# Performance work log

Hardware: AMD Instinct MI355X
Metric: run time of the kernel (lower is better)

## Reference

```python
import jax, jax.numpy as jnp
import numpy as np

N = 4096
IN_F = 128
OUT_F = 128
H = 4
D = OUT_F // H  # head_out = 32
SLOPE = 0.2
LN_EPS = 1e-5


def setup_inputs() -> dict:
    key = jax.random.key(0)
    k_x, k_adj, k_W, k_a = jax.random.split(key, 4)
    x = jax.random.normal(k_x, (N, IN_F), dtype=jnp.float32)
    adjacency = jax.random.randint(k_adj, (N, N), 0, 2).astype(jnp.bool_)
    # xavier-uniform-ish init scales
    w_std = float(np.sqrt(2.0 / (IN_F + H * D)))
    a_std = float(np.sqrt(2.0 / (H + 2 * D)))
    W = jax.random.normal(k_W, (H * D, IN_F), dtype=jnp.float32) * w_std  # torch Linear weight layout
    a = jax.random.normal(k_a, (H, 2 * D), dtype=jnp.float32) * a_std
    ln_gamma = jnp.ones((OUT_F,), dtype=jnp.float32)
    ln_beta = jnp.zeros((OUT_F,), dtype=jnp.float32)
    return {"x": x, "adjacency": adjacency, "W": W, "a": a,
            "ln_gamma": ln_gamma, "ln_beta": ln_beta}


def reference(x, adjacency, W, a, ln_gamma, ln_beta):
    # Wx: (N, H, D)
    Wx = (x @ W.T).reshape(N, H, D)
    # e[i,j,h] = leaky_relu( <Wx[i,h], a[h,:D]> + <Wx[j,h], a[h,D:]> )
    # (exact factorization of the original cat([Wx_i, Wx_j]) * a sum)
    alpha_i = jnp.einsum('nhd,hd->nh', Wx, a[:, :D])  # source/i term
    alpha_j = jnp.einsum('nhd,hd->nh', Wx, a[:, D:])  # neighbor/j term
    e = alpha_i[:, None, :] + alpha_j[None, :, :]      # (N, N, H)
    e = jnp.where(e >= 0, e, SLOPE * e)                # LeakyReLU
    e = jnp.where(adjacency[:, :, None], e, -jnp.inf)  # mask non-edges
    attn = jax.nn.softmax(e, axis=1)                   # softmax over j
    out = jnp.einsum('ijh,jhd->ihd', attn, Wx).reshape(N, H * D)
    y = out + x                                        # residual (dims match)
    mu = jnp.mean(y, axis=-1, keepdims=True)
    var = jnp.mean((y - mu) ** 2, axis=-1, keepdims=True)
    return ln_gamma * (y - mu) / jnp.sqrt(var + LN_EPS) + ln_beta
```

## Files before the change

### kernel.cpp

```cpp
#include <hip/hip_runtime.h>
#include <hip/hip_bf16.h>
#include <stdint.h>

#define NN 4096
#define SLOPE 0.2f
#define LOG2E 1.44269504088896340736f

typedef float f32x4 __attribute__((ext_vector_type(4)));
typedef float f32x2 __attribute__((ext_vector_type(2)));
typedef short s16x8 __attribute__((ext_vector_type(8)));
typedef unsigned u32x4 __attribute__((ext_vector_type(4)));

static __device__ __forceinline__ unsigned f32_to_bf16_rne(float f) {
    unsigned u = __builtin_bit_cast(unsigned, f);
    return (u + 0x7FFFu + ((u >> 16) & 1u)) >> 16;
}

__global__ __launch_bounds__(256) void k0_pack(const unsigned* __restrict__ src,
                                               unsigned* __restrict__ bits) {
    __shared__ int s_i32;
    const int t = threadIdx.x;
    if (t == 0) {
        int all_small = 1;
        for (int i = 0; i < 32; ++i) all_small &= (src[i] <= 1u);
        s_i32 = all_small;
    }
    __syncthreads();
    const long o = (long)blockIdx.x * 256 + t;
    unsigned m = 0;
    if (s_i32) {
        const u32x4* p = (const u32x4*)src + o * 8;
        #pragma unroll
        for (int g = 0; g < 8; ++g) {
            u32x4 v = p[g];
            m |= (v.x & 1u) << (g * 4) | (v.y & 1u) << (g * 4 + 1) |
                 (v.z & 1u) << (g * 4 + 2) | (v.w & 1u) << (g * 4 + 3);
        }
    } else {
        const u32x4* p = (const u32x4*)src + o * 2;
        #pragma unroll
        for (int g = 0; g < 2; ++g) {
            u32x4 v = p[g];
            unsigned d[4] = {v.x, v.y, v.z, v.w};
            #pragma unroll
            for (int q = 0; q < 4; ++q)
                #pragma unroll
                for (int b = 0; b < 4; ++b)
                    m |= ((d[q] >> (8 * b)) & 1u) << (g * 16 + q * 4 + b);
        }
    }
    bits[o] = m;
}

__global__ __launch_bounds__(256) void k1_wx(const float* __restrict__ x,
                                             const float* __restrict__ W,
                                             const float* __restrict__ a,
                                             unsigned short* __restrict__ wxb,
                                             float* __restrict__ ai_s,
                                             float* __restrict__ ajT_s) {
    __shared__ unsigned short WL[128 * 136];
    __shared__ unsigned short XL[16 * 136];
    __shared__ float WxF[16 * 132];

    const int t = threadIdx.x;
    const int i0 = blockIdx.x * 16;

    for (int p = t; p < 8192; p += 256) {
        f32x2 w2 = *(const f32x2*)(W + 2 * p);
        unsigned lo = f32_to_bf16_rne(w2.x);
        unsigned hi = f32_to_bf16_rne(w2.y);
        int c = (2 * p) >> 7, k = (2 * p) & 127;
        *(unsigned*)&WL[c * 136 + k] = lo | (hi << 16);
    }
    for (int p = t; p < 1024; p += 256) {
        f32x2 x2 = *(const f32x2*)(x + (long)i0 * 128 + 2 * p);
        unsigned lo = f32_to_bf16_rne(x2.x);
        unsigned hi = f32_to_bf16_rne(x2.y);
        int r = (2 * p) >> 7, k = (2 * p) & 127;
        *(unsigned*)&XL[r * 136 + k] = lo | (hi << 16);
    }
    __syncthreads();

    const int w = t >> 6, l = t & 63, m = l & 15, q = l >> 4;
    f32x4 acc0 = {0.f, 0.f, 0.f, 0.f}, acc1 = {0.f, 0.f, 0.f, 0.f};
    #pragma unroll
    for (int ks = 0; ks < 4; ++ks) {
        s16x8 af = *(const s16x8*)&XL[m * 136 + ks * 32 + q * 8];
        s16x8 b0 = *(const s16x8*)&WL[(w * 32 + m) * 136 + ks * 32 + q * 8];
        s16x8 b1 = *(const s16x8*)&WL[(w * 32 + 16 + m) * 136 + ks * 32 + q * 8];
        acc0 = __builtin_amdgcn_mfma_f32_16x16x32_bf16(af, b0, acc0, 0, 0, 0);
        acc1 = __builtin_amdgcn_mfma_f32_16x16x32_bf16(af, b1, acc1, 0, 0, 0);
    }
    #pragma unroll
    for (int j2 = 0; j2 < 2; ++j2) {
        const int fblk = 2 * w + j2;
        f32x4 acc = j2 ? acc1 : acc0;
        #pragma unroll
        for (int reg = 0; reg < 4; ++reg) {
            float v = acc[reg];
            int row_g = i0 + q * 4 + reg;
            int kl = row_g & 31, jblk = row_g >> 5;
            wxb[(((jblk * 8 + fblk) * 64 + (kl >> 3) * 16 + m) << 3) + (kl & 7)] =
                (unsigned short)f32_to_bf16_rne(v);
            WxF[(q * 4 + reg) * 132 + fblk * 16 + m] = v;
        }
    }
    __syncthreads();
    if (t < 64) {
        int r = t >> 2, h = t & 3;
        float s_i = 0.f, s_j = 0.f;
        const float* ar = a + h * 64;
        #pragma unroll
        for (int d = 0; d < 32; ++d) {
            float wv = WxF[r * 132 + h * 32 + d];
            s_i += wv * ar[d];
            s_j += wv * ar[32 + d];
        }
        ai_s[(i0 + r) * 4 + h] = s_i * LOG2E;
        ajT_s[h * NN + i0 + r] = s_j * LOG2E;
    }
}

__global__ __launch_bounds__(512) void k2_attn(const float* __restrict__ x,
                                               const unsigned* __restrict__ adjbits,
                                               const unsigned short* __restrict__ wxb,
                                               const float* __restrict__ ai_s,
                                               const float* __restrict__ ajT_s,
                                               const float* __restrict__ gamma,
                                               const float* __restrict__ beta,
                                               float* __restrict__ out) {
    __shared__ float C_lds[4][16][32];
    __shared__ float l_lds[4][16];

    const int t = threadIdx.x;
    const int i0 = blockIdx.x * 16;
    const int w = t >> 6, l = t & 63;
    const int h = w & 3, p = w >> 2;
    const int m = l & 15, q = l >> 4;
    const int rg = i0 + m;

    const float ai = ai_s[rg * 4 + h];
    const unsigned* abp = adjbits + (long)rg * 128;
    const float* ajp = ajT_s + h * NN + q * 8;
    const unsigned short* bp = wxb + ((2 * h) * 64 + l) * 8;

    f32x4 acc0 = {0.f, 0.f, 0.f, 0.f}, acc1 = {0.f, 0.f, 0.f, 0.f};
    float lpart = 0.f;

    for (int ks = p; ks < 128; ks += 2) {
        unsigned mq = (abp[ks] >> (q * 8)) & 0xffu;
        f32x4 aj0 = *(const f32x4*)(ajp + ks * 32);
        f32x4 aj1 = *(const f32x4*)(ajp + ks * 32 + 4);
        s16x8 b0 = *(const s16x8*)(bp + ks * 4096);
        s16x8 b1 = *(const s16x8*)(bp + ks * 4096 + 512);

        float ev[8];
        #pragma unroll
        for (int e = 0; e < 8; ++e) {
            float s = ai + (e < 4 ? aj0[e] : aj1[e - 4]);
            s = fmaxf(s, SLOPE * s);
            float ex = __builtin_amdgcn_exp2f(s);
            float msk = (float)((mq >> e) & 1u);
            ex *= msk;
            lpart += ex;
            ev[e] = ex;
        }
        union { s16x8 v; unsigned u[4]; } af;
        #pragma unroll
        for (int pr = 0; pr < 4; ++pr) {
            unsigned e0 = __builtin_bit_cast(unsigned, ev[2 * pr]);
            unsigned e1 = __builtin_bit_cast(unsigned, ev[2 * pr + 1]);
            af.u[pr] = __builtin_amdgcn_perm(e1, e0, 0x07060302);
        }
        acc0 = __builtin_amdgcn_mfma_f32_16x16x32_bf16(af.v, b0, acc0, 0, 0, 0);
        acc1 = __builtin_amdgcn_mfma_f32_16x16x32_bf16(af.v, b1, acc1, 0, 0, 0);
    }

    lpart += __shfl_xor(lpart, 16, 64);
    lpart += __shfl_xor(lpart, 32, 64);

    if (p == 0) {
        #pragma unroll
        for (int reg = 0; reg < 4; ++reg) {
            C_lds[h][q * 4 + reg][m] = acc0[reg];
            C_lds[h][q * 4 + reg][16 + m] = acc1[reg];
        }
        if (l < 16) l_lds[h][l] = lpart;
    }
    __syncthreads();
    if (p == 1) {
        #pragma unroll
        for (int reg = 0; reg < 4; ++reg) {
            C_lds[h][q * 4 + reg][m] += acc0[reg];
            C_lds[h][q * 4 + reg][16 + m] += acc1[reg];
        }
        if (l < 16) l_lds[h][l] += lpart;
    }
    __syncthreads();

    {
        const int r = t >> 5, c32 = t & 31;
        const int f0 = c32 * 4;
        const int hh = f0 >> 5, cl = f0 & 31;
        const float linv = 1.0f / l_lds[hh][r];
        f32x4 xv = *(const f32x4*)(x + (long)(i0 + r) * 128 + f0);
        float y[4], s1 = 0.f, s2 = 0.f;
        #pragma unroll
        for (int kk = 0; kk < 4; ++kk) {
            float yy = C_lds[hh][r][cl + kk] * linv + xv[kk];
            y[kk] = yy; s1 += yy; s2 += yy * yy;
        }
        #pragma unroll
        for (int s = 1; s <= 16; s <<= 1) {
            s1 += __shfl_xor(s1, s, 64);
            s2 += __shfl_xor(s2, s, 64);
        }
        const float mean = s1 * (1.0f / 128.0f);
        const float var = s2 * (1.0f / 128.0f) - mean * mean;
        const float rstd = rsqrtf(var + 1e-5f);
        f32x4 gv = *(const f32x4*)(gamma + f0);
        f32x4 bv = *(const f32x4*)(beta + f0);
        f32x4 ov;
        #pragma unroll
        for (int kk = 0; kk < 4; ++kk)
            ov[kk] = gv[kk] * ((y[kk] - mean) * rstd) + bv[kk];
        *(f32x4*)(out + (long)(i0 + r) * 128 + f0) = ov;
    }
}

extern "C" void kernel_launch(void* const* d_in, const int* in_sizes, int n_in,
                              void* d_out, int out_size, void* d_ws, size_t ws_size,
                              hipStream_t stream) {
    const float* x = (const float*)d_in[0];
    const unsigned* adj_raw = (const unsigned*)d_in[1];
    const float* W = (const float*)d_in[2];
    const float* a = (const float*)d_in[3];
    const float* gamma = (const float*)d_in[4];
    const float* beta = (const float*)d_in[5];

    unsigned short* wxb = (unsigned short*)d_ws;
    float* ai_s = (float*)((char*)d_ws + (1 << 20));
    float* ajT_s = (float*)((char*)d_ws + (1 << 20) + (64 << 10));
    unsigned* adjbits = (unsigned*)((char*)d_ws + (2 << 20));

    k0_pack<<<2048, 256, 0, stream>>>(adj_raw, adjbits);
    k1_wx<<<256, 256, 0, stream>>>(x, W, a, wxb, ai_s, ajT_s);
    k2_attn<<<256, 512, 0, stream>>>(x, adjbits, wxb, ai_s, ajT_s, gamma, beta,
                                     (float*)d_out);
}
```

Before: 150.2 us.

## Double k2 block to 1024 threads and stage neighbor scores and mask in LDS

The attention kernel now runs 16 waves per block, with each head's key range split four ways instead of two. All per-head neighbor scores and the block's adjacency bit rows are staged in shared memory before the main loop. The partial results from the four splits are merged serially in LDS. The intent is more latency hiding and fewer repeated global loads, at the cost of a 64KB+ LDS footprint limiting occupancy and extra barriers. The wx kernel's bf16 conversion loops are also widened to 128-bit loads with 64-bit LDS stores, and the mask multiply becomes a select.

After: 136.4 us. -9.2%, faster.

```diff
diff --git a/kernel.cpp b/kernel.cpp
--- a/kernel.cpp
+++ b/kernel.cpp
@@ -65,19 +65,21 @@
     const int t = threadIdx.x;
     const int i0 = blockIdx.x * 16;
 
-    for (int p = t; p < 8192; p += 256) {
-        f32x2 w2 = *(const f32x2*)(W + 2 * p);
-        unsigned lo = f32_to_bf16_rne(w2.x);
-        unsigned hi = f32_to_bf16_rne(w2.y);
-        int c = (2 * p) >> 7, k = (2 * p) & 127;
-        *(unsigned*)&WL[c * 136 + k] = lo | (hi << 16);
-    }
-    for (int p = t; p < 1024; p += 256) {
-        f32x2 x2 = *(const f32x2*)(x + (long)i0 * 128 + 2 * p);
-        unsigned lo = f32_to_bf16_rne(x2.x);
-        unsigned hi = f32_to_bf16_rne(x2.y);
-        int r = (2 * p) >> 7, k = (2 * p) & 127;
-        *(unsigned*)&XL[r * 136 + k] = lo | (hi << 16);
+    for (int p4 = t; p4 < 4096; p4 += 256) {
+        f32x4 w4 = *(const f32x4*)(W + 4 * p4);
+        unsigned lo = f32_to_bf16_rne(w4.x) | (f32_to_bf16_rne(w4.y) << 16);
+        unsigned hi = f32_to_bf16_rne(w4.z) | (f32_to_bf16_rne(w4.w) << 16);
+        int c = (4 * p4) >> 7, k = (4 * p4) & 127;
+        *(unsigned long long*)&WL[c * 136 + k] =
+            (unsigned long long)lo | ((unsigned long long)hi << 32);
+    }
+    for (int p4 = t; p4 < 512; p4 += 256) {
+        f32x4 x4 = *(const f32x4*)(x + (long)i0 * 128 + 4 * p4);
+        unsigned lo = f32_to_bf16_rne(x4.x) | (f32_to_bf16_rne(x4.y) << 16);
+        unsigned hi = f32_to_bf16_rne(x4.z) | (f32_to_bf16_rne(x4.w) << 16);
+        int r = (4 * p4) >> 7, k = (4 * p4) & 127;
+        *(unsigned long long*)&XL[r * 136 + k] =
+            (unsigned long long)lo | ((unsigned long long)hi << 32);
     }
     __syncthreads();
 
@@ -121,14 +123,17 @@
     }
 }
 
-__global__ __launch_bounds__(512) void k2_attn(const float* __restrict__ x,
-                                               const unsigned* __restrict__ adjbits,
-                                               const unsigned short* __restrict__ wxb,
-                                               const float* __restrict__ ai_s,
-                                               const float* __restrict__ ajT_s,
-                                               const float* __restrict__ gamma,
-                                               const float* __restrict__ beta,
-                                               float* __restrict__ out) {
+__global__ __launch_bounds__(1024, 4) void k2_attn(
+        const float* __restrict__ x,
+        const unsigned* __restrict__ adjbits,
+        const unsigned short* __restrict__ wxb,
+        const float* __restrict__ ai_s,
+        const float* __restrict__ ajT_s,
+        const float* __restrict__ gamma,
+        const float* __restrict__ beta,
+        float* __restrict__ out) {
+    __shared__ float ajL[4][4096];
+    __shared__ unsigned maskL[16][132];
     __shared__ float C_lds[4][16][32];
     __shared__ float l_lds[4][16];
 
@@ -137,20 +142,34 @@
     const int w = t >> 6, l = t & 63;
     const int h = w & 3, p = w >> 2;
     const int m = l & 15, q = l >> 4;
-    const int rg = i0 + m;
-
-    const float ai = ai_s[rg * 4 + h];
-    const unsigned* abp = adjbits + (long)rg * 128;
-    const float* ajp = ajT_s + h * NN + q * 8;
+
+    {
+        const f32x4* src = (const f32x4*)ajT_s;
+        f32x4* dst = (f32x4*)&ajL[0][0];
+        #pragma unroll
+        for (int g = 0; g < 4; ++g) dst[t + 1024 * g] = src[t + 1024 * g];
+    }
+    {
+        #pragma unroll
+        for (int g = 0; g < 2; ++g) {
+            int idx = t + 1024 * g;
+            int r = idx >> 7, c = idx & 127;
+            maskL[r][c] = adjbits[(long)(i0 + r) * 128 + c];
+        }
+    }
+    const float ai = ai_s[(i0 + m) * 4 + h];
+    __syncthreads();
+
     const unsigned short* bp = wxb + ((2 * h) * 64 + l) * 8;
+    const float* ajh = &ajL[h][0] + q * 8;
 
     f32x4 acc0 = {0.f, 0.f, 0.f, 0.f}, acc1 = {0.f, 0.f, 0.f, 0.f};
     float lpart = 0.f;
 
-    for (int ks = p; ks < 128; ks += 2) {
-        unsigned mq = (abp[ks] >> (q * 8)) & 0xffu;
-        f32x4 aj0 = *(const f32x4*)(ajp + ks * 32);
-        f32x4 aj1 = *(const f32x4*)(ajp + ks * 32 + 4);
+    for (int ks = p; ks < 128; ks += 4) {
+        unsigned mq = (maskL[m][ks] >> (q * 8)) & 0xffu;
+        f32x4 aj0 = *(const f32x4*)(ajh + ks * 32);
+        f32x4 aj1 = *(const f32x4*)(ajh + ks * 32 + 4);
         s16x8 b0 = *(const s16x8*)(bp + ks * 4096);
         s16x8 b1 = *(const s16x8*)(bp + ks * 4096 + 512);
 
@@ -160,8 +179,7 @@
             float s = ai + (e < 4 ? aj0[e] : aj1[e - 4]);
             s = fmaxf(s, SLOPE * s);
             float ex = __builtin_amdgcn_exp2f(s);
-            float msk = (float)((mq >> e) & 1u);
-            ex *= msk;
+            ex = ((mq >> e) & 1u) ? ex : 0.0f;
             lpart += ex;
             ev[e] = ex;
         }
@@ -197,8 +215,26 @@
         if (l < 16) l_lds[h][l] += lpart;
     }
     __syncthreads();
-
-    {
+    if (p == 2) {
+        #pragma unroll
+        for (int reg = 0; reg < 4; ++reg) {
+            C_lds[h][q * 4 + reg][m] += acc0[reg];
+            C_lds[h][q * 4 + reg][16 + m] += acc1[reg];
+        }
+        if (l < 16) l_lds[h][l] += lpart;
+    }
+    __syncthreads();
+    if (p == 3) {
+        #pragma unroll
+        for (int reg = 0; reg < 4; ++reg) {
+            C_lds[h][q * 4 + reg][m] += acc0[reg];
+            C_lds[h][q * 4 + reg][16 + m] += acc1[reg];
+        }
+        if (l < 16) l_lds[h][l] += lpart;
+    }
+    __syncthreads();
+
+    if (t < 512) {
         const int r = t >> 5, c32 = t & 31;
         const int f0 = c32 * 4;
         const int hh = f0 >> 5, cl = f0 & 31;
@@ -245,6 +281,6 @@
 
     k0_pack<<<2048, 256, 0, stream>>>(adj_raw, adjbits);
     k1_wx<<<256, 256, 0, stream>>>(x, W, a, wxb, ai_s, ajT_s);
-    k2_attn<<<256, 512, 0, stream>>>(x, adjbits, wxb, ai_s, ajT_s, gamma, beta,
-                                     (float*)d_out);
-}
+    k2_attn<<<256, 1024, 0, stream>>>(x, adjbits, wxb, ai_s, ajT_s, gamma, beta,
+                                      (float*)d_out);
+}
```
